# Kernel optimization log

Hardware: AMD Instinct MI355X
Metric: run time of the kernel (lower is better)

The kernel has to match this reference:

```python
import jax, jax.numpy as jnp
import numpy as np

N_NODES, N_EDGES, B, NGRID = 8000, 64000, 64, 12
HID, BAS, L, DEG = 128, 128, 3, 3
IN_S, IN_V, OUT_S, OUT_V, WIDE = 16, 2, 8, 1, 4
RADIUS = 1000.0


def fibonacci_sphere(n):
    # deterministic near-uniform S2 grid (stand-in for uniform_grid_s2)
    i = jnp.arange(n, dtype=jnp.float32)
    golden = (1.0 + 5.0 ** 0.5) / 2.0
    theta = 2.0 * jnp.pi * i / golden
    z = 1.0 - (2.0 * i + 1.0) / n
    r = jnp.sqrt(jnp.maximum(1.0 - z * z, 0.0))
    return jnp.stack([r * jnp.cos(theta), r * jnp.sin(theta), z], axis=-1)


def poly_features(x, degree):
    # PolynomialFeatures: cat of x, x(x)x flattened, ... up to given degree
    feats, cur = [x], x
    for _ in range(1, degree):
        cur = (cur[..., :, None] * x[..., None, :]).reshape(x.shape[:-1] + (-1,))
        feats.append(cur)
    return jnp.concatenate(feats, axis=-1)


def gelu(t):
    return jax.nn.gelu(t, approximate=False)


def setup_inputs():
    key = jax.random.key(0)
    ks = jax.random.split(key, 20)
    def w(k, shape, fan_in):
        return jax.random.normal(k, shape, dtype=jnp.float32) / np.float32(np.sqrt(fan_in))
    x = jax.random.normal(ks[0], (N_NODES, IN_S), dtype=jnp.float32)
    vec = jax.random.normal(ks[1], (N_NODES, IN_V, 3), dtype=jnp.float32)
    pos = jax.random.normal(ks[2], (N_NODES, 3), dtype=jnp.float32) * 3.0
    Q = jax.random.orthogonal(ks[3], 3, shape=(B,), dtype=jnp.float32)
    Q = Q * jnp.sign(jnp.linalg.det(Q))[:, None, None]  # proper rotations
    edge_index = jax.random.randint(ks[4], (2, N_EDGES), 0, N_NODES)
    batch = jnp.sort(jax.random.randint(ks[5], (N_NODES,), 0, B))
    d_sp, d_sh = 14, 3  # poly features of dim-2 and dim-1 attrs at degree 3
    return dict(
        x=x, vec=vec, pos=pos, rand_SO3=Q,
        Wsp1=w(ks[6], (d_sp, HID), d_sp), bsp1=jnp.zeros((HID,), jnp.float32),
        Wsp2=w(ks[7], (HID, BAS), HID), bsp2=jnp.zeros((BAS,), jnp.float32),
        Wsh1=w(ks[8], (d_sh, HID), d_sh), bsh1=jnp.zeros((HID,), jnp.float32),
        Wsh2=w(ks[9], (HID, BAS), HID), bsh2=jnp.zeros((BAS,), jnp.float32),
        Wemb=w(ks[10], (IN_S + IN_V, HID), IN_S + IN_V),
        Wk=w(ks[11], (L, BAS, HID), BAS), Wfk=w(ks[12], (L, BAS, HID), BAS),
        bconv=jnp.zeros((L, HID), jnp.float32),
        ln_g=jnp.ones((L, HID), jnp.float32), ln_b=jnp.zeros((L, HID), jnp.float32),
        W1=w(ks[13], (L, HID, WIDE * HID), HID), b1=jnp.zeros((L, WIDE * HID), jnp.float32),
        W2=w(ks[14], (L, WIDE * HID, HID), WIDE * HID), b2=jnp.zeros((L, HID), jnp.float32),
        Wro=w(ks[15], (L, HID, OUT_S + OUT_V), HID), bro=jnp.zeros((L, OUT_S + OUT_V), jnp.float32),
        edge_index=edge_index, batch=batch)


def _forward(x, vec, pos, rand_SO3, Wsp1, bsp1, Wsp2, bsp2, Wsh1, bsh1, Wsh2, bsh2,
             Wemb, Wk, Wfk, bconv, ln_g, ln_b, W1, b1, W2, b2, Wro, bro,
             edge_index, batch):
    grid0 = fibonacci_sphere(NGRID)                       # [n,3]
    grid = jnp.einsum('bij,nj->bni', rand_SO3, grid0)     # [B,n,3] per-graph rotated grid
    node_grid = grid[batch]                               # [N,n,3]
    send, recv = edge_index[0], edge_index[1]
    # lift inputs to the sphere
    xs = jnp.broadcast_to(x[:, None, :], (N_NODES, NGRID, IN_S))      # scalar_to_sphere
    xv = jnp.einsum('bcd,bnd->bnc', vec, node_grid)                   # vec_to_sphere
    f = jnp.concatenate([xs, xv], axis=-1)                # [N,n,IN_S+IN_V]
    # invariant spatial attributes per edge/orientation
    rel = (pos[send] - pos[recv])[:, None, :]             # [E,1,3]
    g_r = node_grid[recv]                                 # [E,n,3]
    inv1 = jnp.sum(rel * g_r, axis=-1, keepdims=True)     # parallel component
    inv2 = jnp.linalg.norm(rel - inv1 * g_r, axis=-1, keepdims=True)  # orthogonal dist
    attr_sp = jnp.concatenate([inv1, inv2], axis=-1)      # [E,n,2]
    attr_sh = (grid0 @ grid0.T)[..., None]                # [n,n,1] rotation-invariant
    kb_sp = gelu(gelu(poly_features(attr_sp, DEG) @ Wsp1 + bsp1) @ Wsp2 + bsp2)  # [E,n,BAS]
    kb_sh = gelu(gelu(poly_features(attr_sh, DEG) @ Wsh1 + bsh1) @ Wsh2 + bsh2)  # [n,n,BAS]
    # NOTE: the original forward multiplies attr_spatial by a polynomial window AFTER the
    # basis is computed; that result is never used again (dead code), so it is omitted here.
    h = f @ Wemb                                          # [N,n,HID]
    readout = jnp.zeros((N_NODES, NGRID, OUT_S + OUT_V), h.dtype)
    for l in range(L):
        h_in = h
        # depthwise spatial conv via gather-multiply-scatter
        k = kb_sp @ Wk[l]                                 # [E,n,HID]
        msg = h_in[send] * k
        agg = jax.ops.segment_sum(msg, recv, num_segments=N_NODES)    # [N,n,HID]
        # depthwise spherical (fiber) conv
        fk = kb_sh @ Wfk[l]                               # [n,n,HID]
        x2 = jnp.einsum('boc,poc->bpc', agg, fk) / NGRID + bconv[l]
        # LayerNorm + inverted-bottleneck MLP, ConvNeXt residual to block input
        mu = jnp.mean(x2, axis=-1, keepdims=True)
        var = jnp.var(x2, axis=-1, keepdims=True)
        hn = (x2 - mu) * jax.lax.rsqrt(var + 1e-5) * ln_g[l] + ln_b[l]
        mlp = gelu(hn @ W1[l] + b1[l]) @ W2[l] + b2[l]
        h = h_in + mlp
        readout = readout + (h @ Wro[l] + bro[l]) / L
    ro_s, ro_v = readout[..., :OUT_S], readout[..., OUT_S:]
    out_s = jax.ops.segment_sum(jnp.mean(ro_s, axis=-2), batch, num_segments=B)  # [B,OUT_S]
    ov = jnp.einsum('bnc,bnd->bcd', ro_v, node_grid) / NGRID                     # sphere_to_vec
    out_v = jax.ops.segment_sum(ov, batch, num_segments=B)                       # [B,OUT_V,3]
    return out_s, out_v


def reference(x, vec, pos, rand_SO3, Wsp1, bsp1, Wsp2, bsp2, Wsh1, bsh1, Wsh2, bsh2,
              Wemb, Wk, Wfk, bconv, ln_g, ln_b, W1, b1, W2, b2, Wro, bro,
              edge_index, batch):
    return _forward(x, vec, pos, rand_SO3, Wsp1, bsp1, Wsp2, bsp2, Wsh1, bsh1, Wsh2, bsh2,
                    Wemb, Wk, Wfk, bconv, ln_g, ln_b, W1, b1, W2, b2, Wro, bro,
                    edge_index, batch)
```

## Files before the change

### kernel.cpp

```cpp
#include <hip/hip_runtime.h>
#include <hip/hip_bf16.h>

#define N_NODES 8000
#define N_EDGES 64000
#define NBATCH  64
#define NGRID   12
#define HIDC    128
#define MNPB    8
#define EB      64
#define SE      8
#define NBLK    (N_EDGES / EB)

typedef __bf16 bf16x8 __attribute__((ext_vector_type(8)));
typedef __bf16 bf16x4 __attribute__((ext_vector_type(4)));
typedef float  f32x4  __attribute__((ext_vector_type(4)));
typedef int    i32x4  __attribute__((ext_vector_type(4)));

__device__ __forceinline__ float gelu_f(float x) {
    float u = 0.7978845608f * x * (1.0f + 0.044715f * x * x);
    float e = __expf(2.0f * u);
    float r = __builtin_amdgcn_rcpf(e + 1.0f);
    return x * (1.0f - r);
}

__global__ void k_grid(const float* __restrict__ Q, float* __restrict__ grid0,
                       float* __restrict__ grid) {
    int t = threadIdx.x;
    __shared__ float g0[12][3];
    if (t < 12) {
        float fi = (float)t;
        float theta = 6.28318530717958647692f * fi / 1.61803398874989484820f;
        float z = 1.0f - (2.0f * fi + 1.0f) / 12.0f;
        float r = sqrtf(fmaxf(1.0f - z * z, 0.0f));
        g0[t][0] = r * cosf(theta);
        g0[t][1] = r * sinf(theta);
        g0[t][2] = z;
        grid0[t * 3 + 0] = g0[t][0];
        grid0[t * 3 + 1] = g0[t][1];
        grid0[t * 3 + 2] = g0[t][2];
    }
    __syncthreads();
    for (int idx = t; idx < NBATCH * 12 * 3; idx += blockDim.x) {
        int b = idx / 36, rmd = idx % 36, n = rmd / 3, i = rmd % 3;
        float acc = 0.f;
        #pragma unroll
        for (int j = 0; j < 3; ++j) acc += Q[b * 9 + i * 3 + j] * g0[n][j];
        grid[idx] = acc;
    }
}

__global__ __launch_bounds__(128) void k_kbsh(
    const float* __restrict__ grid0,
    const float* __restrict__ Wsh1, const float* __restrict__ bsh1,
    const float* __restrict__ Wsh2, const float* __restrict__ bsh2,
    const float* __restrict__ Wfk, float* __restrict__ fk) {
    int row = blockIdx.x;
    int p = row / 12, o = row % 12, t = threadIdx.x;
    float tt = grid0[p*3]*grid0[o*3] + grid0[p*3+1]*grid0[o*3+1] + grid0[p*3+2]*grid0[o*3+2];
    float p1 = tt, p2 = tt * tt, p3 = p2 * tt;
    float h1 = gelu_f(p1 * Wsh1[t] + p2 * Wsh1[128 + t] + p3 * Wsh1[256 + t] + bsh1[t]);
    __shared__ float h1S[128];
    __shared__ float h2S[128];
    h1S[t] = h1;
    __syncthreads();
    float acc = bsh2[t];
    #pragma unroll 8
    for (int k = 0; k < 128; ++k) acc += h1S[k] * Wsh2[k * 128 + t];
    h2S[t] = gelu_f(acc);
    __syncthreads();
    for (int l = 0; l < 3; ++l) {
        float a = 0.f;
        #pragma unroll 8
        for (int k = 0; k < 128; ++k) a += h2S[k] * Wfk[l * 16384 + k * 128 + t];
        fk[l * 18432 + (p * 128 + t) * 12 + o] = a;
    }
}

__global__ __launch_bounds__(128) void k_embed(
    const float* __restrict__ x, const float* __restrict__ vec,
    const int* __restrict__ batch, const float* __restrict__ grid,
    const float* __restrict__ Wemb, float* __restrict__ node_grid,
    __bf16* __restrict__ h_bf) {
    __shared__ float WembS[18 * 128];
    __shared__ float ngS[36];
    __shared__ float xS[16];
    __shared__ float vS[6];
    int n = blockIdx.x, t = threadIdx.x;
    for (int i = t; i < 18 * 128; i += 128) WembS[i] = Wemb[i];
    int b = batch[n];
    if (t < 36) { float g = grid[b * 36 + t]; ngS[t] = g; node_grid[n * 36 + t] = g; }
    if (t < 16) xS[t] = x[n * 16 + t];
    if (t >= 16 && t < 22) vS[t - 16] = vec[n * 6 + (t - 16)];
    __syncthreads();
    for (int g = 0; g < NGRID; ++g) {
        float g0 = ngS[g*3], g1 = ngS[g*3+1], g2 = ngS[g*3+2];
        float xv0 = vS[0]*g0 + vS[1]*g1 + vS[2]*g2;
        float xv1 = vS[3]*g0 + vS[4]*g1 + vS[5]*g2;
        float acc = xv0 * WembS[16*128 + t] + xv1 * WembS[17*128 + t];
        #pragma unroll
        for (int j = 0; j < 16; ++j) acc += xS[j] * WembS[j*128 + t];
        h_bf[((size_t)n * NGRID + g) * HIDC + t] = (__bf16)acc;
    }
}

__global__ __launch_bounds__(256) void k_deg(const int* __restrict__ recv,
                                             int* __restrict__ deg) {
    int e = blockIdx.x * 256 + threadIdx.x;
    if (e < N_EDGES) atomicAdd(&deg[recv[e]], 1);
}

__global__ __launch_bounds__(1024) void k_scan(const int* __restrict__ deg,
                                               int* __restrict__ rowptr,
                                               int* __restrict__ cursor) {
    __shared__ int part[1024];
    int t = threadIdx.x;
    int base = t * 8;
    int local[8];
    int s = 0;
    #pragma unroll
    for (int j = 0; j < 8; ++j) {
        int idx = base + j;
        int v = (idx < N_NODES) ? deg[idx] : 0;
        local[j] = s;
        s += v;
    }
    part[t] = s;
    __syncthreads();
    for (int off = 1; off < 1024; off <<= 1) {
        int v = (t >= off) ? part[t - off] : 0;
        __syncthreads();
        part[t] += v;
        __syncthreads();
    }
    int excl = (t == 0) ? 0 : part[t - 1];
    #pragma unroll
    for (int j = 0; j < 8; ++j) {
        int idx = base + j;
        if (idx < N_NODES) {
            int v = excl + local[j];
            rowptr[idx] = v;
            cursor[idx] = v;
        }
    }
    if (t == 1023) rowptr[N_NODES] = part[1023];
}

__global__ __launch_bounds__(256) void k_fill(const int* __restrict__ recv,
                                              int* __restrict__ cursor,
                                              int* __restrict__ perm) {
    int e = blockIdx.x * 256 + threadIdx.x;
    if (e < N_EDGES) {
        int r = recv[e];
        int p = atomicAdd(&cursor[r], 1);
        perm[p] = e;
    }
}

__global__ __launch_bounds__(256) void k_attr_sorted(
    const float* __restrict__ pos, const float* __restrict__ ng,
    const int* __restrict__ send, const int* __restrict__ recv,
    const int* __restrict__ perm,
    float* __restrict__ attr_s, int* __restrict__ send_s,
    int* __restrict__ recv_s) {
    int idx = blockIdx.x * 256 + threadIdx.x;
    if (idx >= (N_EDGES + 16) * 12) return;
    int i = idx / 12, g = idx % 12;
    if (i < N_EDGES) {
        int e = perm[i];
        int s = send[e], r = recv[e];
        float rx = pos[s*3+0] - pos[r*3+0];
        float ry = pos[s*3+1] - pos[r*3+1];
        float rz = pos[s*3+2] - pos[r*3+2];
        const float* gr = ng + ((size_t)r * 12 + g) * 3;
        float g0 = gr[0], g1 = gr[1], g2 = gr[2];
        float iv1 = rx*g0 + ry*g1 + rz*g2;
        float wx = rx - iv1*g0, wy = ry - iv1*g1, wz = rz - iv1*g2;
        attr_s[(size_t)idx * 2 + 0] = iv1;
        attr_s[(size_t)idx * 2 + 1] = sqrtf(wx*wx + wy*wy + wz*wz);
        if (g == 0) { send_s[i] = s; recv_s[i] = r; }
    } else {
        attr_s[(size_t)idx * 2 + 0] = 0.f;
        attr_s[(size_t)idx * 2 + 1] = 0.f;
        if (g == 0) { send_s[i] = 0; recv_s[i] = 0; }
    }
}

__global__ __launch_bounds__(256) void k_prepw2(
    const float* __restrict__ Wsp2, const float* __restrict__ Wk,
    const float* __restrict__ W1, const float* __restrict__ W2,
    __bf16* __restrict__ WT) {
    int i = blockIdx.x * 256 + threadIdx.x;
    if (i >= 7 * 65536) return;
    float v;
    if (i < 65536) {
        int buf = i >> 14, r = i & 16383;
        int n = r >> 7, k = r & 127;
        v = (buf == 0) ? Wsp2[k * 128 + n] : Wk[(buf - 1) * 16384 + k * 128 + n];
    } else {
        int i2 = i - 65536;
        int l = i2 >> 16, r = i2 & 65535;
        if (l < 3) {
            int n = r >> 7, k = r & 127;
            v = W1[l * 65536 + k * 512 + n];
        } else {
            int l2 = l - 3;
            int n = r >> 9, k = r & 511;
            v = W2[l2 * 65536 + k * 128 + n];
        }
    }
    WT[i] = (__bf16)v;
}

__global__ __launch_bounds__(128) void k_prepw_i8(
    const float* __restrict__ Wk, signed char* __restrict__ Wk8,
    float* __restrict__ s_c) {
    int i = blockIdx.x * 128 + threadIdx.x;
    if (i >= 384) return;
    int l = i / 128, col = i % 128;
    float mx = 0.f;
    for (int k = 0; k < 128; ++k)
        mx = fmaxf(mx, fabsf(Wk[l * 16384 + k * 128 + col]));
    float s = fmaxf(mx * (1.0f / 127.0f), 1e-20f);
    s_c[i] = s;
    float inv = 127.0f / fmaxf(mx, 1e-20f);
    for (int k = 0; k < 128; ++k) {
        int q = __float2int_rn(Wk[l * 16384 + k * 128 + col] * inv);
        q = q > 127 ? 127 : (q < -127 ? -127 : q);
        Wk8[(size_t)l * 16384 + col * 128 + k] = (signed char)q;
    }
}

__global__ __launch_bounds__(128) void k_prepw_p(
    const float* __restrict__ Wsp1, const float* __restrict__ bsp1,
    __bf16* __restrict__ WP1T) {
    int col = threadIdx.x;
    float w1[14];
    #pragma unroll
    for (int j = 0; j < 14; ++j) w1[j] = Wsp1[j * 128 + col];
    float vals[10];
    vals[0] = w1[0];
    vals[1] = w1[1];
    vals[2] = w1[2];
    vals[3] = w1[3] + w1[4];
    vals[4] = w1[5];
    vals[5] = w1[6];
    vals[6] = w1[7] + w1[8] + w1[10];
    vals[7] = w1[9] + w1[11] + w1[12];
    vals[8] = w1[13];
    vals[9] = bsp1[col];
    for (int k = 0; k < 32; ++k)
        WP1T[col * 32 + k] = (k < 10) ? (__bf16)vals[k] : (__bf16)0.f;
}

__global__ __launch_bounds__(192) void k_prepw_ro(
    const float* __restrict__ Wro, __bf16* __restrict__ WroF) {
    int t = threadIdx.x;
    int l = t / 64, lane = t % 64;
    int l15 = lane & 15, quad = lane >> 4;
    #pragma unroll
    for (int ks = 0; ks < 4; ++ks)
        #pragma unroll
        for (int j = 0; j < 8; ++j) {
            int k = ks * 32 + quad * 8 + j;
            float v = (l15 < 9) ? Wro[l * 1152 + k * 9 + l15] : 0.f;
            WroF[(size_t)(l * 64 + lane) * 32 + ks * 8 + j] = (__bf16)v;
        }
}

__global__ __launch_bounds__(256, 4) void k_kb_i8(
    const float* __restrict__ attr_s,
    const __bf16* __restrict__ W2T, const __bf16* __restrict__ WP1T,
    const float* __restrict__ bsp2,
    signed char* __restrict__ kb8, float* __restrict__ s_r) {
    __shared__ __align__(16) __bf16 H1[64 * 136];
    __shared__ __align__(16) signed char K8[64 * 144];
    __shared__ float rowmaxS[64];
    int t = threadIdx.x;
    int lane = t & 63, w = t >> 6, l15 = lane & 15, quad = lane >> 4;
    size_t grow0 = (size_t)blockIdx.x * 64;
    {
        float2 ab = ((const float2*)attr_s)[grow0 + w * 16 + l15];
        float a = ab.x, b = ab.y;
        float aa = a * a, abm = a * b, bb = b * b;
        float m0 = quad == 0 ? a        : (quad == 1 ? bb * b : 0.f);
        float m1 = quad == 0 ? b        : (quad == 1 ? 1.f    : 0.f);
        float m2 = quad == 0 ? aa       : 0.f;
        float m3 = quad == 0 ? abm      : 0.f;
        float m4 = quad == 0 ? bb       : 0.f;
        float m5 = quad == 0 ? aa * a   : 0.f;
        float m6 = quad == 0 ? aa * b   : 0.f;
        float m7 = quad == 0 ? abm * b  : 0.f;
        bf16x8 afrag = { (__bf16)m0, (__bf16)m1, (__bf16)m2, (__bf16)m3,
                         (__bf16)m4, (__bf16)m5, (__bf16)m6, (__bf16)m7 };
        #pragma unroll
        for (int n = 0; n < 8; ++n) {
            bf16x8 bp = *(const bf16x8*)(WP1T + (n * 16 + l15) * 32 + quad * 8);
            f32x4 cacc = {0.f, 0.f, 0.f, 0.f};
            cacc = __builtin_amdgcn_mfma_f32_16x16x32_bf16(afrag, bp, cacc, 0, 0, 0);
            #pragma unroll
            for (int rg = 0; rg < 4; ++rg) {
                int row = w * 16 + quad * 4 + rg;
                H1[row * 136 + n * 16 + l15] = (__bf16)gelu_f(cacc[rg]);
            }
        }
    }
    __syncthreads();
    bf16x8 Bf[2][4];
    #pragma unroll
    for (int j = 0; j < 2; ++j)
        #pragma unroll
        for (int ks = 0; ks < 4; ++ks)
            Bf[j][ks] = *(const bf16x8*)(W2T + (size_t)(w * 32 + j * 16 + l15) * 128 + ks * 32 + quad * 8);
    float b2v[2] = { bsp2[w * 32 + l15], bsp2[w * 32 + 16 + l15] };
    f32x4 acc[4][2];
    #pragma unroll
    for (int mt = 0; mt < 4; ++mt) {
        acc[mt][0] = (f32x4){0.f,0.f,0.f,0.f};
        acc[mt][1] = (f32x4){0.f,0.f,0.f,0.f};
        #pragma unroll
        for (int ks = 0; ks < 4; ++ks) {
            bf16x8 af = *(const bf16x8*)(H1 + (mt * 16 + l15) * 136 + ks * 32 + quad * 8);
            acc[mt][0] = __builtin_amdgcn_mfma_f32_16x16x32_bf16(af, Bf[0][ks], acc[mt][0], 0, 0, 0);
            acc[mt][1] = __builtin_amdgcn_mfma_f32_16x16x32_bf16(af, Bf[1][ks], acc[mt][1], 0, 0, 0);
        }
    }
    float g[4][2][4];
    #pragma unroll
    for (int mt = 0; mt < 4; ++mt)
        #pragma unroll
        for (int j = 0; j < 2; ++j)
            #pragma unroll
            for (int rg = 0; rg < 4; ++rg)
                g[mt][j][rg] = gelu_f(acc[mt][j][rg] + b2v[j]);
    __syncthreads();
    #pragma unroll
    for (int mt = 0; mt < 4; ++mt)
        #pragma unroll
        for (int j = 0; j < 2; ++j)
            #pragma unroll
            for (int rg = 0; rg < 4; ++rg) {
                int row = mt * 16 + quad * 4 + rg;
                H1[row * 136 + w * 32 + j * 16 + l15] = (__bf16)g[mt][j][rg];
            }
    __syncthreads();
    if (t < 64) {
        float mx = 0.f;
        #pragma unroll
        for (int ks = 0; ks < 16; ++ks) {
            bf16x8 xv = *(const bf16x8*)(H1 + t * 136 + ks * 8);
            #pragma unroll
            for (int m = 0; m < 8; ++m) mx = fmaxf(mx, fabsf((float)xv[m]));
        }
        float s = fmaxf(mx * (1.0f / 127.0f), 1e-20f);
        rowmaxS[t] = s;
        s_r[grow0 + t] = s;
    }
    __syncthreads();
    #pragma unroll
    for (int mt = 0; mt < 4; ++mt)
        #pragma unroll
        for (int j = 0; j < 2; ++j)
            #pragma unroll
            for (int rg = 0; rg < 4; ++rg) {
                int row = mt * 16 + quad * 4 + rg;
                float inv = __builtin_amdgcn_rcpf(rowmaxS[row]);
                int q = __float2int_rn(g[mt][j][rg] * inv);
                q = q > 127 ? 127 : (q < -127 ? -127 : q);
                K8[row * 144 + w * 32 + j * 16 + l15] = (signed char)q;
            }
    __syncthreads();
    #pragma unroll
    for (int it = 0; it < 2; ++it) {
        int idx = it * 256 + t;
        int row = idx >> 3, cv = idx & 7;
        *(uint4*)(kb8 + (grow0 + row) * 128 + cv * 16) =
            *(const uint4*)(K8 + row * 144 + cv * 16);
    }
}

__global__ __launch_bounds__(256, 4) void k_gscat2(
    const signed char* __restrict__ kb8, const float* __restrict__ s_r,
    const signed char* __restrict__ Wk8, const float* __restrict__ s_cL,
    const int* __restrict__ send_s, const int* __restrict__ recv_s,
    const int* __restrict__ rowptr, const __bf16* __restrict__ h_bf,
    __bf16* __restrict__ aggb) {
    __shared__ __align__(16) signed char T8[96 * 144];
    __shared__ __align__(16) __bf16 P[96 * 136];
    __shared__ float srS[96];
    int t = threadIdx.x;
    int lane = t & 63, w = t >> 6, l15 = lane & 15, quad = lane >> 4;
    int bid = blockIdx.x;
    int n0, n1;
    {
        if (bid == 0) n0 = 0;
        else {
            int tgt = bid * EB, lo = 0, hi = N_NODES;
            while (lo < hi) { int m = (lo + hi) >> 1; if (rowptr[m] < tgt) lo = m + 1; else hi = m; }
            n0 = lo;
        }
        if (bid == NBLK - 1) n1 = N_NODES;
        else {
            int tgt = (bid + 1) * EB, lo = 0, hi = N_NODES;
            while (lo < hi) { int m = (lo + hi) >> 1; if (rowptr[m] < tgt) lo = m + 1; else hi = m; }
            n1 = lo;
        }
    }
    if (n0 >= n1) return;
    int e0 = rowptr[n0], e1 = rowptr[n1];
    long long Bf[2][4];
    #pragma unroll
    for (int j = 0; j < 2; ++j)
        #pragma unroll
        for (int ks = 0; ks < 4; ++ks)
            Bf[j][ks] = *(const long long*)(Wk8 + (size_t)(w * 32 + j * 16 + l15) * 128 + ks * 32 + quad * 8);
    float sc0 = s_cL[w * 32 + l15], sc1 = s_cL[w * 32 + 16 + l15];
    int c = t & 127, half = t >> 7;
    float acc[6] = {0.f, 0.f, 0.f, 0.f, 0.f, 0.f};
    int cur = (e0 < e1) ? recv_s[e0] : -1;
    for (int et0 = e0; et0 < e1; et0 += SE) {
        int cnt = e1 - et0; if (cnt > SE) cnt = SE;
        int nrows = cnt * 12;
        __syncthreads();
        #pragma unroll
        for (int it = 0; it < 3; ++it) {
            int idx = it * 256 + t;
            if (idx < nrows * 8) {
                int row = idx >> 3, cv = idx & 7;
                *(uint4*)(T8 + row * 144 + cv * 16) =
                    *(const uint4*)(kb8 + ((size_t)et0 * 12 + row) * 128 + cv * 16);
            }
        }
        if (t < nrows) srS[t] = s_r[(size_t)et0 * 12 + t];
        __syncthreads();
        int nrt = (nrows + 15) >> 4;
        for (int rt = 0; rt < nrt; ++rt) {
            i32x4 a0 = (i32x4){0, 0, 0, 0};
            i32x4 a1 = (i32x4){0, 0, 0, 0};
            #pragma unroll
            for (int ks = 0; ks < 4; ++ks) {
                long long a = *(const long long*)(T8 + (rt * 16 + l15) * 144 + ks * 32 + quad * 8);
                a0 = __builtin_amdgcn_mfma_i32_16x16x32_i8(a, Bf[0][ks], a0, 0, 0, 0);
                a1 = __builtin_amdgcn_mfma_i32_16x16x32_i8(a, Bf[1][ks], a1, 0, 0, 0);
            }
            #pragma unroll
            for (int rg = 0; rg < 4; ++rg) {
                int row = rt * 16 + quad * 4 + rg;
                float sr = srS[row];
                P[row * 136 + w * 32 + l15]      = (__bf16)((float)a0[rg] * sr * sc0);
                P[row * 136 + w * 32 + 16 + l15] = (__bf16)((float)a1[rg] * sr * sc1);
            }
        }
        __syncthreads();
        for (int el = 0; el < cnt; ++el) {
            int e = et0 + el;
            int r = recv_s[e];
            if (r != cur) {
                __bf16* op = aggb + ((size_t)cur * 128 + c) * 12 + half * 6;
                #pragma unroll
                for (int j = 0; j < 6; ++j) { op[j] = (__bf16)acc[j]; acc[j] = 0.f; }
                cur = r;
            }
            int s = send_s[e];
            const __bf16* hp = h_bf + (size_t)s * 1536 + half * 6 * 128 + c;
            const __bf16* pp = P + (el * 12 + half * 6) * 136 + c;
            #pragma unroll
            for (int j = 0; j < 6; ++j)
                acc[j] += (float)hp[j * 128] * (float)pp[j * 136];
        }
    }
    if (e0 < e1) {
        __bf16* op = aggb + ((size_t)cur * 128 + c) * 12 + half * 6;
        #pragma unroll
        for (int j = 0; j < 6; ++j) op[j] = (__bf16)acc[j];
    }
    for (int n = n0; n < n1; ++n) {
        if (rowptr[n] == rowptr[n + 1]) {
            __bf16* op = aggb + ((size_t)n * 128 + c) * 12 + half * 6;
            #pragma unroll
            for (int j = 0; j < 6; ++j) op[j] = (__bf16)0.f;
        }
    }
}

__global__ __launch_bounds__(256, 3) void k_mlp(
    const __bf16* __restrict__ aggb, const float* __restrict__ fkl,
    const float* __restrict__ bconv, const float* __restrict__ ln_g,
    const float* __restrict__ ln_b,
    const __bf16* __restrict__ W1T, const float* __restrict__ b1,
    const __bf16* __restrict__ W2T2, const float* __restrict__ b2,
    const __bf16* __restrict__ WroFl, const float* __restrict__ bro,
    __bf16* __restrict__ h_bf, float* __restrict__ readout) {
    __shared__ __align__(16) __bf16 X[96 * 136];
    __shared__ __align__(16) __bf16 H4[96 * 136];
    __shared__ float redS[96][2];
    int t = threadIdx.x;
    int lane = t & 63, w = t >> 6, l15 = lane & 15, quad = lane >> 4;
    int c = t & 127, nh = t >> 7;
    int n0 = blockIdx.x * MNPB;
    float bcv = bconv[c];
    {
        float a2[4][12];
        #pragma unroll
        for (int u = 0; u < 4; ++u) {
            const __bf16* ap = aggb + ((size_t)(n0 + nh + u * 2) * 128 + c) * 12;
            #pragma unroll
            for (int v = 0; v < 3; ++v) {
                bf16x4 pk = *(const bf16x4*)(ap + v * 4);
                #pragma unroll
                for (int j = 0; j < 4; ++j) a2[u][v * 4 + j] = (float)pk[j];
            }
        }
        #pragma unroll 4
        for (int p = 0; p < 12; ++p) {
            const float* fp = fkl + ((size_t)p * 128 + c) * 12;
            float fr[12];
            #pragma unroll
            for (int v = 0; v < 3; ++v) {
                float4 fv = *(const float4*)(fp + v * 4);
                fr[v*4+0] = fv.x; fr[v*4+1] = fv.y; fr[v*4+2] = fv.z; fr[v*4+3] = fv.w;
            }
            #pragma unroll
            for (int u = 0; u < 4; ++u) {
                float s = 0.f;
                #pragma unroll
                for (int o = 0; o < 12; ++o) s += a2[u][o] * fr[o];
                X[((nh + u * 2) * 12 + p) * 136 + c] = (__bf16)(s * (1.0f / 12.0f) + bcv);
            }
        }
    }
    __syncthreads();
    for (int r = w * 24; r < w * 24 + 24; ++r) {
        float v0 = (float)X[r * 136 + lane];
        float v1 = (float)X[r * 136 + 64 + lane];
        float s = v0 + v1, s2 = v0 * v0 + v1 * v1;
        for (int off = 32; off > 0; off >>= 1) {
            s += __shfl_down(s, off);
            s2 += __shfl_down(s2, off);
        }
        if (lane == 0) {
            float mu = s * (1.0f / 128.0f);
            float var = s2 * (1.0f / 128.0f) - mu * mu;
            redS[r][0] = mu;
            redS[r][1] = rsqrtf(var + 1e-5f);
        }
    }
    __syncthreads();
    float gv = ln_g[c], bv = ln_b[c];
    #pragma unroll
    for (int nn = nh; nn < 8; nn += 2)
        #pragma unroll
        for (int p = 0; p < 12; ++p) {
            int r = nn * 12 + p;
            float v = (float)X[r * 136 + c];
            X[r * 136 + c] = (__bf16)((v - redS[r][0]) * redS[r][1] * gv + bv);
        }
    __syncthreads();
    f32x4 acc2[6][2];
    #pragma unroll
    for (int mt = 0; mt < 6; ++mt)
        #pragma unroll
        for (int j = 0; j < 2; ++j) acc2[mt][j] = (f32x4){0.f, 0.f, 0.f, 0.f};
    bf16x8 W1f[2][4];
    #pragma unroll
    for (int nt = 0; nt < 2; ++nt)
        #pragma unroll
        for (int ks = 0; ks < 4; ++ks)
            W1f[nt][ks] = *(const bf16x8*)(W1T + (size_t)(w * 32 + nt * 16 + l15) * 128 + ks * 32 + quad * 8);
    for (int ph = 0; ph < 4; ++ph) {
        if (ph) __syncthreads();
        bf16x8 W2f[2][4];
        #pragma unroll
        for (int j = 0; j < 2; ++j)
            #pragma unroll
            for (int ks = 0; ks < 4; ++ks)
                W2f[j][ks] = *(const bf16x8*)(W2T2 + (size_t)(w * 32 + j * 16 + l15) * 512 + ph * 128 + ks * 32 + quad * 8);
        float bj0 = b1[ph * 128 + w * 32 + l15];
        float bj1 = b1[ph * 128 + w * 32 + 16 + l15];
        #pragma unroll
        for (int mt = 0; mt < 6; ++mt) {
            bf16x8 af[4];
            #pragma unroll
            for (int ks = 0; ks < 4; ++ks)
                af[ks] = *(const bf16x8*)(X + (mt * 16 + l15) * 136 + ks * 32 + quad * 8);
            f32x4 a0 = {0.f, 0.f, 0.f, 0.f};
            f32x4 a1 = {0.f, 0.f, 0.f, 0.f};
            #pragma unroll
            for (int ks = 0; ks < 4; ++ks) {
                a0 = __builtin_amdgcn_mfma_f32_16x16x32_bf16(af[ks], W1f[0][ks], a0, 0, 0, 0);
                a1 = __builtin_amdgcn_mfma_f32_16x16x32_bf16(af[ks], W1f[1][ks], a1, 0, 0, 0);
            }
            #pragma unroll
            for (int rg = 0; rg < 4; ++rg) {
                int row = mt * 16 + quad * 4 + rg;
                H4[row * 136 + w * 32 + l15]      = (__bf16)gelu_f(a0[rg] + bj0);
                H4[row * 136 + w * 32 + 16 + l15] = (__bf16)gelu_f(a1[rg] + bj1);
            }
        }
        if (ph < 3) {
            #pragma unroll
            for (int nt = 0; nt < 2; ++nt)
                #pragma unroll
                for (int ks = 0; ks < 4; ++ks)
                    W1f[nt][ks] = *(const bf16x8*)(W1T + (size_t)((ph + 1) * 128 + w * 32 + nt * 16 + l15) * 128 + ks * 32 + quad * 8);
        }
        __syncthreads();
        #pragma unroll
        for (int mt = 0; mt < 6; ++mt)
            #pragma unroll
            for (int ks = 0; ks < 4; ++ks) {
                bf16x8 af = *(const bf16x8*)(H4 + (mt * 16 + l15) * 136 + ks * 32 + quad * 8);
                acc2[mt][0] = __builtin_amdgcn_mfma_f32_16x16x32_bf16(af, W2f[0][ks], acc2[mt][0], 0, 0, 0);
                acc2[mt][1] = __builtin_amdgcn_mfma_f32_16x16x32_bf16(af, W2f[1][ks], acc2[mt][1], 0, 0, 0);
            }
    }
    #pragma unroll
    for (int mt = 0; mt < 6; ++mt) {
        float bj0 = b2[w * 32 + l15], bj1 = b2[w * 32 + 16 + l15];
        #pragma unroll
        for (int rg = 0; rg < 4; ++rg) {
            int row = mt * 16 + quad * 4 + rg;
            int node = n0 + row / 12, pp = row % 12;
            size_t hi = ((size_t)node * 12 + pp) * 128;
            {
                int col = w * 32 + l15;
                float hv = (float)h_bf[hi + col] + acc2[mt][0][rg] + bj0;
                h_bf[hi + col] = (__bf16)hv;
                X[row * 136 + col] = (__bf16)hv;
            }
            {
                int col = w * 32 + 16 + l15;
                float hv = (float)h_bf[hi + col] + acc2[mt][1][rg] + bj1;
                h_bf[hi + col] = (__bf16)hv;
                X[row * 136 + col] = (__bf16)hv;
            }
        }
    }
    __syncthreads();
    for (int mt2 = w; mt2 < 6; mt2 += 4) {
        const __bf16* wp = WroFl + (size_t)lane * 32;
        f32x4 a = {0.f, 0.f, 0.f, 0.f};
        #pragma unroll
        for (int ks = 0; ks < 4; ++ks) {
            bf16x8 af = *(const bf16x8*)(X + (mt2 * 16 + l15) * 136 + ks * 32 + quad * 8);
            bf16x8 bf = *(const bf16x8*)(wp + ks * 8);
            a = __builtin_amdgcn_mfma_f32_16x16x32_bf16(af, bf, a, 0, 0, 0);
        }
        if (l15 < 9) {
            float bj = bro[l15];
            #pragma unroll
            for (int rg = 0; rg < 4; ++rg) {
                int row = mt2 * 16 + quad * 4 + rg;
                int node = n0 + row / 12, pp = row % 12;
                size_t ri = ((size_t)node * 12 + pp) * 9 + l15;
                readout[ri] += (a[rg] + bj) * (1.0f / 3.0f);
            }
        }
    }
}

__global__ __launch_bounds__(128) void k_out(
    const float* __restrict__ readout, const float* __restrict__ node_grid,
    const int* __restrict__ batch, float* __restrict__ out) {
    int n = blockIdx.x * 128 + threadIdx.x;
    if (n >= N_NODES) return;
    int b = batch[n];
    const float* ro = readout + (size_t)n * 108;
    float ss[8] = {0, 0, 0, 0, 0, 0, 0, 0};
    float v0 = 0.f, v1 = 0.f, v2 = 0.f;
    for (int p = 0; p < 12; ++p) {
        #pragma unroll
        for (int j = 0; j < 8; ++j) ss[j] += ro[p * 9 + j];
        float rv = ro[p * 9 + 8];
        v0 += rv * node_grid[n * 36 + p * 3 + 0];
        v1 += rv * node_grid[n * 36 + p * 3 + 1];
        v2 += rv * node_grid[n * 36 + p * 3 + 2];
    }
    #pragma unroll
    for (int j = 0; j < 8; ++j) atomicAdd(&out[b * 8 + j], ss[j] * (1.0f / 12.0f));
    atomicAdd(&out[512 + b * 3 + 0], v0 * (1.0f / 12.0f));
    atomicAdd(&out[512 + b * 3 + 1], v1 * (1.0f / 12.0f));
    atomicAdd(&out[512 + b * 3 + 2], v2 * (1.0f / 12.0f));
}

extern "C" void kernel_launch(void* const* d_in, const int* in_sizes, int n_in,
                              void* d_out, int out_size, void* d_ws, size_t ws_size,
                              hipStream_t stream) {
    const float* x    = (const float*)d_in[0];
    const float* vec  = (const float*)d_in[1];
    const float* pos  = (const float*)d_in[2];
    const float* Q    = (const float*)d_in[3];
    const float* Wsp1 = (const float*)d_in[4];
    const float* bsp1 = (const float*)d_in[5];
    const float* Wsp2 = (const float*)d_in[6];
    const float* bsp2 = (const float*)d_in[7];
    const float* Wsh1 = (const float*)d_in[8];
    const float* bsh1 = (const float*)d_in[9];
    const float* Wsh2 = (const float*)d_in[10];
    const float* bsh2 = (const float*)d_in[11];
    const float* Wemb = (const float*)d_in[12];
    const float* Wk   = (const float*)d_in[13];
    const float* Wfk  = (const float*)d_in[14];
    const float* bconv= (const float*)d_in[15];
    const float* ln_g = (const float*)d_in[16];
    const float* ln_b = (const float*)d_in[17];
    const float* W1   = (const float*)d_in[18];
    const float* b1   = (const float*)d_in[19];
    const float* W2   = (const float*)d_in[20];
    const float* b2   = (const float*)d_in[21];
    const float* Wro  = (const float*)d_in[22];
    const float* bro  = (const float*)d_in[23];
    const int* ei     = (const int*)d_in[24];
    const int* batch  = (const int*)d_in[25];
    const int* send = ei;
    const int* recv = ei + N_EDGES;

    float* ws = (float*)d_ws;
    float* grid0  = ws;
    float* grid   = ws + 64;
    float* fk     = ws + 2368;
    float* ng     = ws + 57664;
    float* ro     = ws + 345664;
    float* attr_s = ws + 1209664;
    const size_t P_WT  = 2746048;
    const size_t P_WK8 = P_WT + 229376;
    const size_t P_SC  = P_WK8 + 12288;
    const size_t P_WP  = P_SC + 384;
    const size_t P_WROF= P_WP + 2048;
    const size_t P_H   = P_WROF + 3072;
    const size_t P_AGG = P_H + 6144000;
    const size_t P_KB8 = P_AGG + 6144000;
    const size_t P_SR  = P_KB8 + 24576000;
    const size_t T_INT = P_SR + 768000;
    const size_t NEED  = (T_INT + 216096) * 4ull;

    if (ws_size < NEED) return;

    __bf16* WT   = (__bf16*)(ws + P_WT);
    signed char* Wk8 = (signed char*)(ws + P_WK8);
    float* s_c   = ws + P_SC;
    __bf16* WP1T = (__bf16*)(ws + P_WP);
    __bf16* WroF = (__bf16*)(ws + P_WROF);
    __bf16* hA   = (__bf16*)(ws + P_H);
    __bf16* aggb = (__bf16*)(ws + P_AGG);
    signed char* kb8 = (signed char*)(ws + P_KB8);
    float* s_r   = ws + P_SR;
    int*   ibase = (int*)(ws + T_INT);
    int* deg    = ibase;
    int* cursor = ibase + 8000;
    int* rowptr = ibase + 16000;
    int* perm   = ibase + 24064;
    int* send_s = ibase + 88064;
    int* recv_s = ibase + 152080;

    const __bf16* Wsp2T = WT;
    const __bf16* W1T   = WT + 65536;
    const __bf16* W2T   = WT + 65536 + 3 * 65536;

    hipMemsetAsync(d_out, 0, sizeof(float) * (size_t)out_size, stream);
    hipMemsetAsync(ro, 0, sizeof(float) * 864000, stream);
    hipMemsetAsync(deg, 0, sizeof(int) * 8000, stream);

    k_grid<<<1, 256, 0, stream>>>(Q, grid0, grid);
    k_kbsh<<<144, 128, 0, stream>>>(grid0, Wsh1, bsh1, Wsh2, bsh2, Wfk, fk);
    k_embed<<<N_NODES, 128, 0, stream>>>(x, vec, batch, grid, Wemb, ng, hA);
    k_deg<<<250, 256, 0, stream>>>(recv, deg);
    k_scan<<<1, 1024, 0, stream>>>(deg, rowptr, cursor);
    k_fill<<<250, 256, 0, stream>>>(recv, cursor, perm);
    k_attr_sorted<<<((N_EDGES + 16) * 12 + 255) / 256, 256, 0, stream>>>(
        pos, ng, send, recv, perm, attr_s, send_s, recv_s);
    k_prepw2<<<(7 * 65536 + 255) / 256, 256, 0, stream>>>(Wsp2, Wk, W1, W2, WT);
    k_prepw_i8<<<3, 128, 0, stream>>>(Wk, Wk8, s_c);
    k_prepw_p<<<1, 128, 0, stream>>>(Wsp1, bsp1, WP1T);
    k_prepw_ro<<<1, 192, 0, stream>>>(Wro, WroF);

    k_kb_i8<<<N_EDGES * 12 / 64, 256, 0, stream>>>(attr_s, Wsp2T, WP1T, bsp2, kb8, s_r);

    for (int l = 0; l < 3; ++l) {
        k_gscat2<<<NBLK, 256, 0, stream>>>(kb8, s_r,
            Wk8 + (size_t)l * 16384, s_c + l * 128,
            send_s, recv_s, rowptr, hA, aggb);
        k_mlp<<<N_NODES / MNPB, 256, 0, stream>>>(aggb, fk + l * 18432,
            bconv + l * 128, ln_g + l * 128, ln_b + l * 128,
            W1T + l * 65536, b1 + l * 512, W2T + l * 65536, b2 + l * 128,
            WroF + l * 2048, bro + l * 9, hA, ro);
    }
    k_out<<<(N_NODES + 127) / 128, 128, 0, stream>>>(ro, ng, batch, (float*)d_out);
}
```

Baseline: 896.3 us.

## Prefetch next edge tile into registers and parallelize row-max reduction

The edge-conv loop now loads the next chunk of int8 kernel-basis rows and scales into registers while the current chunk is processed with MFMA. This hides global-load latency behind compute, at the cost of extra registers (three uint4 per thread), which may hurt occupancy. The per-row absmax in the kb quantization kernel is now split across all 256 threads with a small shared-memory reduction, replacing the 64-thread serial scan. That costs one extra barrier.

```diff
diff --git a/kernel.cpp b/kernel.cpp
--- a/kernel.cpp
+++ b/kernel.cpp
@@ -275,6 +275,7 @@
     __shared__ __align__(16) __bf16 H1[64 * 136];
     __shared__ __align__(16) signed char K8[64 * 144];
     __shared__ float rowmaxS[64];
+    __shared__ float rm4[64][4];
     int t = threadIdx.x;
     int lane = t & 63, w = t >> 6, l15 = lane & 15, quad = lane >> 4;
     size_t grow0 = (size_t)blockIdx.x * 64;
@@ -343,14 +344,20 @@
                 H1[row * 136 + w * 32 + j * 16 + l15] = (__bf16)g[mt][j][rg];
             }
     __syncthreads();
+    {
+        int row = t & 63, qt = t >> 6;
+        float mx = 0.f;
+        #pragma unroll
+        for (int ks = 0; ks < 4; ++ks) {
+            bf16x8 xv = *(const bf16x8*)(H1 + row * 136 + qt * 32 + ks * 8);
+            #pragma unroll
+            for (int m = 0; m < 8; ++m) mx = fmaxf(mx, fabsf((float)xv[m]));
+        }
+        rm4[row][qt] = mx;
+    }
+    __syncthreads();
     if (t < 64) {
-        float mx = 0.f;
-        #pragma unroll
-        for (int ks = 0; ks < 16; ++ks) {
-            bf16x8 xv = *(const bf16x8*)(H1 + t * 136 + ks * 8);
-            #pragma unroll
-            for (int m = 0; m < 8; ++m) mx = fmaxf(mx, fabsf((float)xv[m]));
-        }
+        float mx = fmaxf(fmaxf(rm4[t][0], rm4[t][1]), fmaxf(rm4[t][2], rm4[t][3]));
         float s = fmaxf(mx * (1.0f / 127.0f), 1e-20f);
         rowmaxS[t] = s;
         s_r[grow0 + t] = s;
@@ -417,21 +424,43 @@
     int c = t & 127, half = t >> 7;
     float acc[6] = {0.f, 0.f, 0.f, 0.f, 0.f, 0.f};
     int cur = (e0 < e1) ? recv_s[e0] : -1;
+    uint4 R0, R1, R2;
+    float Rs = 0.f;
+    bool v0, v1, v2, vs;
+    {
+        int cnt = e1 - e0; if (cnt > SE) cnt = SE;
+        int nr8 = cnt * 96;
+        v0 = t < nr8;
+        v1 = 256 + t < nr8;
+        v2 = 512 + t < nr8;
+        vs = t < cnt * 12;
+        if (v0) { int idx = t;       R0 = *(const uint4*)(kb8 + ((size_t)e0 * 12 + (idx >> 3)) * 128 + (idx & 7) * 16); }
+        if (v1) { int idx = 256 + t; R1 = *(const uint4*)(kb8 + ((size_t)e0 * 12 + (idx >> 3)) * 128 + (idx & 7) * 16); }
+        if (v2) { int idx = 512 + t; R2 = *(const uint4*)(kb8 + ((size_t)e0 * 12 + (idx >> 3)) * 128 + (idx & 7) * 16); }
+        if (vs) Rs = s_r[(size_t)e0 * 12 + t];
+    }
     for (int et0 = e0; et0 < e1; et0 += SE) {
         int cnt = e1 - et0; if (cnt > SE) cnt = SE;
         int nrows = cnt * 12;
         __syncthreads();
-        #pragma unroll
-        for (int it = 0; it < 3; ++it) {
-            int idx = it * 256 + t;
-            if (idx < nrows * 8) {
-                int row = idx >> 3, cv = idx & 7;
-                *(uint4*)(T8 + row * 144 + cv * 16) =
-                    *(const uint4*)(kb8 + ((size_t)et0 * 12 + row) * 128 + cv * 16);
-            }
-        }
-        if (t < nrows) srS[t] = s_r[(size_t)et0 * 12 + t];
+        if (v0) { int idx = t;       *(uint4*)(T8 + (idx >> 3) * 144 + (idx & 7) * 16) = R0; }
+        if (v1) { int idx = 256 + t; *(uint4*)(T8 + (idx >> 3) * 144 + (idx & 7) * 16) = R1; }
+        if (v2) { int idx = 512 + t; *(uint4*)(T8 + (idx >> 3) * 144 + (idx & 7) * 16) = R2; }
+        if (vs) srS[t] = Rs;
         __syncthreads();
+        int net0 = et0 + SE;
+        if (net0 < e1) {
+            int ncnt = e1 - net0; if (ncnt > SE) ncnt = SE;
+            int nr8 = ncnt * 96;
+            v0 = t < nr8;
+            v1 = 256 + t < nr8;
+            v2 = 512 + t < nr8;
+            vs = t < ncnt * 12;
+            if (v0) { int idx = t;       R0 = *(const uint4*)(kb8 + ((size_t)net0 * 12 + (idx >> 3)) * 128 + (idx & 7) * 16); }
+            if (v1) { int idx = 256 + t; R1 = *(const uint4*)(kb8 + ((size_t)net0 * 12 + (idx >> 3)) * 128 + (idx & 7) * 16); }
+            if (v2) { int idx = 512 + t; R2 = *(const uint4*)(kb8 + ((size_t)net0 * 12 + (idx >> 3)) * 128 + (idx & 7) * 16); }
+            if (vs) Rs = s_r[(size_t)net0 * 12 + t];
+        }
         int nrt = (nrows + 15) >> 4;
         for (int rt = 0; rt < nrt; ++rt) {
             i32x4 a0 = (i32x4){0, 0, 0, 0};
```

Result: no change. 880.2 us (-1.8%).
